# Optimization experiments

Measured on AMD Instinct MI355X. Metric: run time of the kernel, lower is better.

Reference implementation:

```python
import jax, jax.numpy as jnp
import numpy as np

N_NODES = 50000
N_EDGES = 800000
D_IN = 128
D_OUT = 128
D_RED = 32  # out_features // reduction
ORDER = 3


def setup_inputs() -> dict:
    key = jax.random.key(0)
    ks = jax.random.split(key, 16)
    s = 1.0 / np.sqrt(D_IN)
    inp = {
        'features': jax.random.normal(ks[0], (N_NODES, D_IN), jnp.float32),
        'edge_row': jax.random.randint(ks[1], (N_EDGES,), 0, N_NODES, jnp.int32),
        'edge_col': jax.random.randint(ks[2], (N_EDGES,), 0, N_NODES, jnp.int32),
        'edge_val': jax.random.uniform(ks[3], (N_EDGES,), jnp.float32) / 16.0,  # ~1/avg_degree normalization
        'w1': jax.random.normal(ks[4], (D_IN, D_OUT), jnp.float32) * s,
        'b1': jax.random.normal(ks[5], (D_OUT,), jnp.float32) * s,
        'w2': jax.random.normal(ks[6], (D_IN, D_OUT), jnp.float32) * s,
        'b2': jax.random.normal(ks[7], (D_OUT,), jnp.float32) * s,
        'w3': jax.random.normal(ks[8], (D_IN, D_OUT), jnp.float32) * s,
        'b3': jax.random.normal(ks[9], (D_OUT,), jnp.float32) * s,
        'fc1_w': jax.random.normal(ks[10], (D_OUT, D_RED), jnp.float32) * s,
        'fc1_b': jax.random.normal(ks[11], (D_RED,), jnp.float32) * s,
        'fc2_w': jax.random.normal(ks[12], (D_RED, D_OUT), jnp.float32) * (1.0 / np.sqrt(D_RED)),
        'fc2_b': jax.random.normal(ks[13], (D_OUT,), jnp.float32) * s,
    }
    return inp


def reference(features, edge_row, edge_col, edge_val, w1, b1, w2, b2, w3, b3,
              fc1_w, fc1_b, fc2_w, fc2_b):
    def spmm(x):  # sparse [N,N] @ dense [N,D] via gather + segment_sum
        msgs = edge_val[:, None] * x[edge_col]          # [E, D]
        return jax.ops.segment_sum(msgs, edge_row, num_segments=N_NODES)

    def ngnn(w, b, order):
        h = jnp.tanh(features @ w)                      # active=True path
        for _ in range(order):                          # order spmm hops
            h = spmm(h)
        return h + b

    abstract = [ngnn(w, b, k + 1) for k, (w, b) in enumerate([(w1, b1), (w2, b2), (w3, b3)])]
    feats = jnp.stack(abstract, axis=0)                 # [order, N, D]
    m = jnp.mean(feats, axis=1)                         # [order, D]
    a = jax.nn.relu(m @ fc1_w + fc1_b) @ fc2_w + fc2_b  # [order, D]
    a = jax.nn.softmax(a, axis=0)                       # softmax over order dim
    out = jnp.einsum('ond,od->nd', feats, a)            # weighted combine
    return out
```

## Files before the change

kernel.cpp:

```cpp
#include <hip/hip_runtime.h>
#include <cstdint>

#define N_NODES 50000
#define N_EDGES 800000
#define DIM 128
#define EPCAP 64

typedef _Float16 half8 __attribute__((ext_vector_type(8)));
typedef float f32x4 __attribute__((ext_vector_type(4)));


__device__ inline unsigned pack_half2(float lo, float hi) {
    union { _Float16 h[2]; unsigned u; } cv;
    cv.h[0] = (_Float16)lo; cv.h[1] = (_Float16)hi;
    return cv.u;
}
__device__ inline float h_lo(unsigned u) {
    union { unsigned u; _Float16 h[2]; } cv; cv.u = u; return (float)cv.h[0];
}
__device__ inline float h_hi(unsigned u) {
    union { unsigned u; _Float16 h[2]; } cv; cv.u = u; return (float)cv.h[1];
}


__global__ void scatter_kernel(const int* __restrict__ rows, const int* __restrict__ cols,
                               const float* __restrict__ vals, int* __restrict__ cnt,
                               unsigned* __restrict__ ep, int ne) {
    int e = blockIdx.x * blockDim.x + threadIdx.x;
    if (e < ne) {
        int r = rows[e];
        int p = atomicAdd(&cnt[r], 1);
        union { _Float16 h; unsigned short s; } cv; cv.h = (_Float16)vals[e];
        if (p < EPCAP) ep[(size_t)r * EPCAP + p] = ((unsigned)cv.s << 16) | (unsigned)cols[e];
    }
}


__global__ __launch_bounds__(256) void wprep_kernel(const float* __restrict__ w3,
                                                    const float* __restrict__ w2,
                                                    const float* __restrict__ w1,
                                                    _Float16* __restrict__ Wt) {
    const float* W = (blockIdx.x == 0) ? w3 : (blockIdx.x == 1) ? w2 : w1;
    _Float16* O = Wt + (size_t)blockIdx.x * 16384;
    int tid = threadIdx.x;
    for (int i = tid; i < 16384; i += 256) {
        int j = i >> 7, d = i & 127;
        O[j * 128 + d] = (_Float16)W[d * 128 + j];
    }
}


__global__ __launch_bounds__(256) void gemm_mfma3_kernel(const float* __restrict__ F,
                                                         const _Float16* __restrict__ Wt,
                                                         unsigned* __restrict__ T1, int nrows) {
    __shared__ _Float16 Fs[64 * 128];
    __shared__ _Float16 Ws[128 * 128];
    int tid = threadIdx.x;
    int lane = tid & 63, wv = tid >> 6;
    int c = lane & 15, g = lane >> 4;
    int rowbase = blockIdx.x * 64;

    for (int i = tid; i < 4096; i += 256) {
        int r = i >> 6;
        int row = rowbase + r; if (row >= nrows) row = nrows - 1;
        float2 fv = ((const float2*)F)[(size_t)row * 64 + (i & 63)];
        *(unsigned*)((char*)Fs + ((i * 4) ^ ((r & 15) << 4))) = pack_half2(fv.x, fv.y);
    }
    __syncthreads();

    half8 afr[4];
    #pragma unroll
    for (int ks = 0; ks < 4; ++ks) {
        int off = (((wv * 16 + c) * 128 + ks * 32 + g * 8) * 2) ^ (c << 4);
        afr[ks] = *(const half8*)((const char*)Fs + off);
    }

    for (int b = 0; b < 3; ++b) {
        const unsigned* WtU = (const unsigned*)(Wt + (size_t)b * 16384);
        for (int i = tid; i < 8192; i += 256) {
            int j = i >> 6;
            *(unsigned*)((char*)Ws + ((i * 4) ^ ((j & 15) << 4))) = WtU[i];
        }
        __syncthreads();

        f32x4 zero = {0.f, 0.f, 0.f, 0.f};
        f32x4 acc[8];
        #pragma unroll
        for (int t = 0; t < 8; ++t) acc[t] = zero;

        #pragma unroll
        for (int ks = 0; ks < 4; ++ks) {
            #pragma unroll
            for (int t = 0; t < 8; ++t) {
                int j = t * 16 + c;
                int off = ((j * 128 + ks * 32 + g * 8) * 2) ^ ((j & 15) << 4);
                half8 bfr = *(const half8*)((const char*)Ws + off);
                acc[t] = __builtin_amdgcn_mfma_f32_16x16x32_f16(afr[ks], bfr, acc[t], 0, 0, 0);
            }
        }

        #pragma unroll
        for (int t = 0; t < 4; ++t) {
            int j = t * 16 + c;
            #pragma unroll
            for (int r = 0; r < 4; ++r) {
                int row = rowbase + wv * 16 + g * 4 + r;
                if (row < nrows)
                    T1[(size_t)row * 192 + b * 64 + j] =
                        pack_half2(tanhf(acc[t][r]), tanhf(acc[t + 4][r]));
            }
        }
        __syncthreads();
    }
}


template <int NCHUNK, bool F32FINAL>
__global__ __launch_bounds__(512) void spmm_stage_kernel(const int* __restrict__ cnts,
                                                         const unsigned* __restrict__ ep,
                                                         const unsigned* __restrict__ x,
                                                         unsigned* __restrict__ ob0,
                                                         unsigned* __restrict__ obf,
                                                         float* __restrict__ fout,
                                                         float* __restrict__ csum) {
    __shared__ float cs[128];
    int tid = threadIdx.x;
    if (tid < 128) cs[tid] = 0.f;
    __syncthreads();

    int row = blockIdx.x * 8 + (tid >> 6);
    int lane = tid & 63;
    int n = __builtin_amdgcn_readfirstlane(cnts[row]);
    n = n < EPCAP ? n : EPCAP;
    const unsigned* e0 = ep + (size_t)row * EPCAP;

    float ax[NCHUNK], ay[NCHUNK];
    #pragma unroll
    for (int cc = 0; cc < NCHUNK; ++cc) { ax[cc] = 0.f; ay[cc] = 0.f; }

    const unsigned* xl = x + lane;
    constexpr int U = (NCHUNK == 1) ? 8 : 4;
    int i = 0;
    for (; i + U <= n; i += U) {
        unsigned p[U];
        #pragma unroll
        for (int u = 0; u < U; ++u) p[u] = e0[i + u];
        unsigned gx[U][NCHUNK];
        #pragma unroll
        for (int u = 0; u < U; ++u) {
            unsigned b = (p[u] & 0xFFFFu) * (unsigned)(NCHUNK * 64);
            #pragma unroll
            for (int cc = 0; cc < NCHUNK; ++cc) gx[u][cc] = xl[b + cc * 64];
        }
        #pragma unroll
        for (int u = 0; u < U; ++u) {
            union { unsigned short s; _Float16 h; } cu; cu.s = (unsigned short)(p[u] >> 16);
            float v = (float)cu.h;
            #pragma unroll
            for (int cc = 0; cc < NCHUNK; ++cc) {
                ax[cc] += v * h_lo(gx[u][cc]);
                ay[cc] += v * h_hi(gx[u][cc]);
            }
        }
    }
    for (; i < n; ++i) {
        unsigned p = e0[i];
        unsigned b = (p & 0xFFFFu) * (unsigned)(NCHUNK * 64);
        union { unsigned short s; _Float16 h; } cu; cu.s = (unsigned short)(p >> 16);
        float v = (float)cu.h;
        #pragma unroll
        for (int cc = 0; cc < NCHUNK; ++cc) {
            unsigned gg = xl[b + cc * 64];
            ax[cc] += v * h_lo(gg);
            ay[cc] += v * h_hi(gg);
        }
    }

    #pragma unroll
    for (int cc = 0; cc < NCHUNK - 1; ++cc)
        ob0[(size_t)row * ((NCHUNK - 1) * 64) + cc * 64 + lane] = pack_half2(ax[cc], ay[cc]);

    float fx = ax[NCHUNK - 1], fy = ay[NCHUNK - 1];
    if (F32FINAL) {
        fout[(size_t)row * 128 + lane] = fx;
        fout[(size_t)row * 128 + 64 + lane] = fy;
    } else {
        obf[(size_t)row * 64 + lane] = pack_half2(fx, fy);
    }
    atomicAdd(&cs[2 * lane + 0], fx);
    atomicAdd(&cs[2 * lane + 1], fy);
    __syncthreads();
    if (tid < 128) atomicAdd(&csum[(blockIdx.x & 7) * 384 + tid], cs[tid]);
}


__global__ __launch_bounds__(128) void fc_softmax_kernel(const float* __restrict__ csum,
                                                         const float* __restrict__ b1,
                                                         const float* __restrict__ b2,
                                                         const float* __restrict__ b3,
                                                         const float* __restrict__ fc1w,
                                                         const float* __restrict__ fc1b,
                                                         const float* __restrict__ fc2w,
                                                         const float* __restrict__ fc2b,
                                                         float* __restrict__ wgt) {
    __shared__ float m[3][128];
    __shared__ float r[3][32];
    int t = threadIdx.x;
    const float inv = 1.0f / (float)N_NODES;
    int slot = (t < 64) ? (2 * t) : (2 * (t - 64) + 1);
    #pragma unroll
    for (int k = 0; k < 3; ++k) {
        float s = 0.f;
        #pragma unroll
        for (int rep = 0; rep < 8; ++rep) s += csum[rep * 384 + k * 128 + slot];
        const float* bk = (k == 0) ? b1 : (k == 1) ? b2 : b3;
        m[k][t] = s * inv + bk[t];
    }
    __syncthreads();
    if (t < 96) {
        int k = t >> 5, j = t & 31;
        float acc = fc1b[j];
        for (int d = 0; d < 128; ++d) acc += m[k][d] * fc1w[d * 32 + j];
        r[k][j] = fmaxf(acc, 0.f);
    }
    __syncthreads();
    float a[3];
    #pragma unroll
    for (int k = 0; k < 3; ++k) {
        float acc = fc2b[t];
        for (int j = 0; j < 32; ++j) acc += r[k][j] * fc2w[j * 128 + t];
        a[k] = acc;
    }
    float mx = fmaxf(a[0], fmaxf(a[1], a[2]));
    float e0 = expf(a[0] - mx), e1 = expf(a[1] - mx), e2 = expf(a[2] - mx);
    float s = e0 + e1 + e2;
    wgt[0 * 128 + t] = e0 / s;
    wgt[1 * 128 + t] = e1 / s;
    wgt[2 * 128 + t] = e2 / s;
}


__global__ __launch_bounds__(256) void combine_kernel(float* __restrict__ out,
                                                      const unsigned* __restrict__ f2,
                                                      const unsigned* __restrict__ f3,
                                                      const float* __restrict__ b1,
                                                      const float* __restrict__ b2,
                                                      const float* __restrict__ b3,
                                                      const float* __restrict__ wgt) {
    const int total = N_NODES * 32;
    int idx0 = blockIdx.x * blockDim.x + threadIdx.x;
    int stride = gridDim.x * blockDim.x;
    int qb = idx0 & 31;
    float4 W0 = ((const float4*)wgt)[qb];
    float4 W1 = ((const float4*)wgt)[32 + qb];
    float4 W2 = ((const float4*)wgt)[64 + qb];
    float4 B1 = ((const float4*)b1)[qb];
    float4 B2 = ((const float4*)b2)[qb];
    float4 B3 = ((const float4*)b3)[qb];
    bool hi = qb >= 16;
    int qm = qb & 15;
    for (int idx = idx0; idx < total; idx += stride) {
        int row = idx >> 5;
        float4 v1 = ((const float4*)out)[idx];
        uint4 u2 = ((const uint4*)f2)[row * 16 + qm];
        uint4 u3 = ((const uint4*)f3)[row * 16 + qm];
        float f2x = hi ? h_hi(u2.x) : h_lo(u2.x);
        float f2y = hi ? h_hi(u2.y) : h_lo(u2.y);
        float f2z = hi ? h_hi(u2.z) : h_lo(u2.z);
        float f2w = hi ? h_hi(u2.w) : h_lo(u2.w);
        float f3x = hi ? h_hi(u3.x) : h_lo(u3.x);
        float f3y = hi ? h_hi(u3.y) : h_lo(u3.y);
        float f3z = hi ? h_hi(u3.z) : h_lo(u3.z);
        float f3w = hi ? h_hi(u3.w) : h_lo(u3.w);
        float4 o;
        o.x = (v1.x + B1.x) * W0.x + (f2x + B2.x) * W1.x + (f3x + B3.x) * W2.x;
        o.y = (v1.y + B1.y) * W0.y + (f2y + B2.y) * W1.y + (f3y + B3.y) * W2.y;
        o.z = (v1.z + B1.z) * W0.z + (f2z + B2.z) * W1.z + (f3z + B3.z) * W2.z;
        o.w = (v1.w + B1.w) * W0.w + (f2w + B2.w) * W1.w + (f3w + B3.w) * W2.w;
        ((float4*)out)[idx] = o;
    }
}


extern "C" void kernel_launch(void* const* d_in, const int* in_sizes, int n_in,
                              void* d_out, int out_size, void* d_ws, size_t ws_size,
                              hipStream_t stream) {
    const float* F    = (const float*)d_in[0];
    const int*   erow = (const int*)d_in[1];
    const int*   ecol = (const int*)d_in[2];
    const float* eval_ = (const float*)d_in[3];
    const float* w1 = (const float*)d_in[4];  const float* b1 = (const float*)d_in[5];
    const float* w2 = (const float*)d_in[6];  const float* b2 = (const float*)d_in[7];
    const float* w3 = (const float*)d_in[8];  const float* b3 = (const float*)d_in[9];
    const float* fc1w = (const float*)d_in[10]; const float* fc1b = (const float*)d_in[11];
    const float* fc2w = (const float*)d_in[12]; const float* fc2b = (const float*)d_in[13];
    float* out = (float*)d_out;

    char* ws = (char*)d_ws;
    size_t off = 0;
    auto alloc = [&](size_t bytes) -> void* {
        off = (off + 255) & ~(size_t)255;
        void* p = ws + off;
        off += bytes;
        return p;
    };
    unsigned* T1   = (unsigned*)alloc((size_t)N_NODES * 192 * 4);
    unsigned* T2   = (unsigned*)alloc((size_t)N_NODES * 128 * 4);
    unsigned* T3   = (unsigned*)alloc((size_t)N_NODES * 64 * 4);
    unsigned* ep   = (unsigned*)alloc((size_t)N_NODES * EPCAP * 4);
    int*   counts  = (int*)alloc((size_t)N_NODES * sizeof(int));
    _Float16* Wt   = (_Float16*)alloc(3 * 16384 * sizeof(_Float16));
    float* csum    = (float*)alloc(8 * 3 * 128 * sizeof(float));
    float* wgt     = (float*)alloc(3 * 128 * sizeof(float));
    unsigned* f2bf = T1;
    unsigned* f3bf = T1 + (size_t)N_NODES * 64;

    hipMemsetAsync(counts, 0, (size_t)N_NODES * sizeof(int), stream);
    hipMemsetAsync(csum, 0, 8 * 3 * 128 * sizeof(float), stream);

    scatter_kernel<<<(N_EDGES + 255) / 256, 256, 0, stream>>>(erow, ecol, eval_, counts, ep, N_EDGES);
    wprep_kernel<<<3, 256, 0, stream>>>(w3, w2, w1, Wt);
    gemm_mfma3_kernel<<<(N_NODES + 63) / 64, 256, 0, stream>>>(F, Wt, T1, N_NODES);

    const int spmmGrid = N_NODES / 8;

    spmm_stage_kernel<3, true><<<spmmGrid, 512, 0, stream>>>(counts, ep, T1, T2,
                                                             nullptr, out, csum + 0 * 128);
    spmm_stage_kernel<2, false><<<spmmGrid, 512, 0, stream>>>(counts, ep, T2, T3,
                                                              f2bf, nullptr, csum + 1 * 128);
    spmm_stage_kernel<1, false><<<spmmGrid, 512, 0, stream>>>(counts, ep, T3, nullptr,
                                                              f3bf, nullptr, csum + 2 * 128);

    fc_softmax_kernel<<<1, 128, 0, stream>>>(csum, b1, b2, b3, fc1w, fc1b, fc2w, fc2b, wgt);
    combine_kernel<<<2048, 256, 0, stream>>>(out, f2bf, f3bf, b1, b2, b3, wgt);
}
```

Before: 345.4 us.

## Interleave SpMM feature chunks per lane and fuse small setup kernels

Changes the T1 layout so each lane's three (and two) chunks sit next to each other, letting SpMM gathers use one vector load per edge instead of several strided loads. Unroll is raised to 8 for all stages. The scatter kernel is fused with the weight-transpose kernel using nontemporal stores, the two memsets are merged into one, and the fc/softmax step is folded into every combine block. The fold makes each of the 2048 blocks redo the tiny MLP, which adds redundant work in exchange for fewer launches.

```diff
diff --git a/kernel.cpp b/kernel.cpp
--- a/kernel.cpp
+++ b/kernel.cpp
@@ -23,30 +23,33 @@
 }
 
 
-__global__ void scatter_kernel(const int* __restrict__ rows, const int* __restrict__ cols,
-                               const float* __restrict__ vals, int* __restrict__ cnt,
-                               unsigned* __restrict__ ep, int ne) {
-    int e = blockIdx.x * blockDim.x + threadIdx.x;
-    if (e < ne) {
-        int r = rows[e];
-        int p = atomicAdd(&cnt[r], 1);
-        union { _Float16 h; unsigned short s; } cv; cv.h = (_Float16)vals[e];
-        if (p < EPCAP) ep[(size_t)r * EPCAP + p] = ((unsigned)cv.s << 16) | (unsigned)cols[e];
-    }
-}
-
-
-__global__ __launch_bounds__(256) void wprep_kernel(const float* __restrict__ w3,
-                                                    const float* __restrict__ w2,
-                                                    const float* __restrict__ w1,
-                                                    _Float16* __restrict__ Wt) {
-    const float* W = (blockIdx.x == 0) ? w3 : (blockIdx.x == 1) ? w2 : w1;
-    _Float16* O = Wt + (size_t)blockIdx.x * 16384;
-    int tid = threadIdx.x;
-    for (int i = tid; i < 16384; i += 256) {
-        int j = i >> 7, d = i & 127;
-        O[j * 128 + d] = (_Float16)W[d * 128 + j];
-    }
+__global__ __launch_bounds__(256) void scatter_wprep_kernel(const int* __restrict__ rows,
+                                                            const int* __restrict__ cols,
+                                                            const float* __restrict__ vals,
+                                                            int* __restrict__ cnt,
+                                                            unsigned* __restrict__ ep,
+                                                            const float* __restrict__ w3,
+                                                            const float* __restrict__ w2,
+                                                            const float* __restrict__ w1,
+                                                            _Float16* __restrict__ Wt) {
+    int bx = blockIdx.x;
+    if (bx >= 3125) {
+        int b = bx - 3125;
+        const float* W = (b == 0) ? w3 : (b == 1) ? w2 : w1;
+        _Float16* O = Wt + (size_t)b * 16384;
+        for (int i = threadIdx.x; i < 16384; i += 256) {
+            int j = i >> 7, d = i & 127;
+            O[j * 128 + d] = (_Float16)W[d * 128 + j];
+        }
+        return;
+    }
+    int e = bx * 256 + threadIdx.x;
+    int r = rows[e];
+    int p = atomicAdd(&cnt[r], 1);
+    union { _Float16 h; unsigned short s; } cv; cv.h = (_Float16)vals[e];
+    if (p < EPCAP)
+        __builtin_nontemporal_store(((unsigned)cv.s << 16) | (unsigned)cols[e],
+                                    &ep[(size_t)r * EPCAP + p]);
 }
 
 
@@ -106,7 +109,7 @@
             for (int r = 0; r < 4; ++r) {
                 int row = rowbase + wv * 16 + g * 4 + r;
                 if (row < nrows)
-                    T1[(size_t)row * 192 + b * 64 + j] =
+                    T1[(size_t)row * 192 + j * 3 + b] =
                         pack_half2(tanhf(acc[t][r]), tanhf(acc[t + 4][r]));
             }
         }
@@ -138,19 +141,26 @@
     #pragma unroll
     for (int cc = 0; cc < NCHUNK; ++cc) { ax[cc] = 0.f; ay[cc] = 0.f; }
 
-    const unsigned* xl = x + lane;
-    constexpr int U = (NCHUNK == 1) ? 8 : 4;
+    const unsigned* xl = x + lane * NCHUNK;
+    constexpr int U = 8;
     int i = 0;
     for (; i + U <= n; i += U) {
         unsigned p[U];
         #pragma unroll
         for (int u = 0; u < U; ++u) p[u] = e0[i + u];
-        unsigned gx[U][NCHUNK];
+        unsigned g[U][NCHUNK];
         #pragma unroll
         for (int u = 0; u < U; ++u) {
-            unsigned b = (p[u] & 0xFFFFu) * (unsigned)(NCHUNK * 64);
-            #pragma unroll
-            for (int cc = 0; cc < NCHUNK; ++cc) gx[u][cc] = xl[b + cc * 64];
+            size_t b = (size_t)(p[u] & 0xFFFFu) * (NCHUNK * 64);
+            if constexpr (NCHUNK == 3) {
+                uint3 v = *(const uint3*)(xl + b);
+                g[u][0] = v.x; g[u][1] = v.y; g[u][2] = v.z;
+            } else if constexpr (NCHUNK == 2) {
+                uint2 v = *(const uint2*)(xl + b);
+                g[u][0] = v.x; g[u][1] = v.y;
+            } else {
+                g[u][0] = xl[b];
+            }
         }
         #pragma unroll
         for (int u = 0; u < U; ++u) {
@@ -158,27 +168,32 @@
             float v = (float)cu.h;
             #pragma unroll
             for (int cc = 0; cc < NCHUNK; ++cc) {
-                ax[cc] += v * h_lo(gx[u][cc]);
-                ay[cc] += v * h_hi(gx[u][cc]);
+                ax[cc] += v * h_lo(g[u][cc]);
+                ay[cc] += v * h_hi(g[u][cc]);
             }
         }
     }
     for (; i < n; ++i) {
         unsigned p = e0[i];
-        unsigned b = (p & 0xFFFFu) * (unsigned)(NCHUNK * 64);
+        size_t b = (size_t)(p & 0xFFFFu) * (NCHUNK * 64);
         union { unsigned short s; _Float16 h; } cu; cu.s = (unsigned short)(p >> 16);
         float v = (float)cu.h;
         #pragma unroll
         for (int cc = 0; cc < NCHUNK; ++cc) {
-            unsigned gg = xl[b + cc * 64];
+            unsigned gg = xl[b + cc];
             ax[cc] += v * h_lo(gg);
             ay[cc] += v * h_hi(gg);
         }
     }
 
-    #pragma unroll
-    for (int cc = 0; cc < NCHUNK - 1; ++cc)
-        ob0[(size_t)row * ((NCHUNK - 1) * 64) + cc * 64 + lane] = pack_half2(ax[cc], ay[cc]);
+    if constexpr (NCHUNK == 3) {
+        uint2 o;
+        o.x = pack_half2(ax[0], ay[0]);
+        o.y = pack_half2(ax[1], ay[1]);
+        *(uint2*)(ob0 + (size_t)row * 128 + lane * 2) = o;
+    } else if constexpr (NCHUNK == 2) {
+        ob0[(size_t)row * 64 + lane] = pack_half2(ax[0], ay[0]);
+    }
 
     float fx = ax[NCHUNK - 1], fy = ay[NCHUNK - 1];
     if (F32FINAL) {
@@ -194,66 +209,66 @@
 }
 
 
-__global__ __launch_bounds__(128) void fc_softmax_kernel(const float* __restrict__ csum,
-                                                         const float* __restrict__ b1,
-                                                         const float* __restrict__ b2,
-                                                         const float* __restrict__ b3,
-                                                         const float* __restrict__ fc1w,
-                                                         const float* __restrict__ fc1b,
-                                                         const float* __restrict__ fc2w,
-                                                         const float* __restrict__ fc2b,
-                                                         float* __restrict__ wgt) {
+__global__ __launch_bounds__(256) void combine_kernel(float* __restrict__ out,
+                                                      const unsigned* __restrict__ f2,
+                                                      const unsigned* __restrict__ f3,
+                                                      const float* __restrict__ csum,
+                                                      const float* __restrict__ b1,
+                                                      const float* __restrict__ b2,
+                                                      const float* __restrict__ b3,
+                                                      const float* __restrict__ fc1w,
+                                                      const float* __restrict__ fc1b,
+                                                      const float* __restrict__ fc2w,
+                                                      const float* __restrict__ fc2b) {
     __shared__ float m[3][128];
-    __shared__ float r[3][32];
+    __shared__ float rr[3][32];
+    __shared__ float wgt[3][128];
     int t = threadIdx.x;
-    const float inv = 1.0f / (float)N_NODES;
-    int slot = (t < 64) ? (2 * t) : (2 * (t - 64) + 1);
-    #pragma unroll
-    for (int k = 0; k < 3; ++k) {
-        float s = 0.f;
-        #pragma unroll
-        for (int rep = 0; rep < 8; ++rep) s += csum[rep * 384 + k * 128 + slot];
-        const float* bk = (k == 0) ? b1 : (k == 1) ? b2 : b3;
-        m[k][t] = s * inv + bk[t];
+
+    if (t < 128) {
+        const float inv = 1.0f / (float)N_NODES;
+        int slot = (t < 64) ? (2 * t) : (2 * (t - 64) + 1);
+        #pragma unroll
+        for (int k = 0; k < 3; ++k) {
+            float s = 0.f;
+            #pragma unroll
+            for (int rep = 0; rep < 8; ++rep) s += csum[rep * 384 + k * 128 + slot];
+            const float* bk = (k == 0) ? b1 : (k == 1) ? b2 : b3;
+            m[k][t] = s * inv + bk[t];
+        }
     }
     __syncthreads();
     if (t < 96) {
         int k = t >> 5, j = t & 31;
         float acc = fc1b[j];
         for (int d = 0; d < 128; ++d) acc += m[k][d] * fc1w[d * 32 + j];
-        r[k][j] = fmaxf(acc, 0.f);
-    }
-    __syncthreads();
-    float a[3];
-    #pragma unroll
-    for (int k = 0; k < 3; ++k) {
-        float acc = fc2b[t];
-        for (int j = 0; j < 32; ++j) acc += r[k][j] * fc2w[j * 128 + t];
-        a[k] = acc;
-    }
-    float mx = fmaxf(a[0], fmaxf(a[1], a[2]));
-    float e0 = expf(a[0] - mx), e1 = expf(a[1] - mx), e2 = expf(a[2] - mx);
-    float s = e0 + e1 + e2;
-    wgt[0 * 128 + t] = e0 / s;
-    wgt[1 * 128 + t] = e1 / s;
-    wgt[2 * 128 + t] = e2 / s;
-}
-
-
-__global__ __launch_bounds__(256) void combine_kernel(float* __restrict__ out,
-                                                      const unsigned* __restrict__ f2,
-                                                      const unsigned* __restrict__ f3,
-                                                      const float* __restrict__ b1,
-                                                      const float* __restrict__ b2,
-                                                      const float* __restrict__ b3,
-                                                      const float* __restrict__ wgt) {
+        rr[k][j] = fmaxf(acc, 0.f);
+    }
+    __syncthreads();
+    if (t < 128) {
+        float a[3];
+        #pragma unroll
+        for (int k = 0; k < 3; ++k) {
+            float acc = fc2b[t];
+            for (int j = 0; j < 32; ++j) acc += rr[k][j] * fc2w[j * 128 + t];
+            a[k] = acc;
+        }
+        float mx = fmaxf(a[0], fmaxf(a[1], a[2]));
+        float e0 = expf(a[0] - mx), e1 = expf(a[1] - mx), e2 = expf(a[2] - mx);
+        float s = e0 + e1 + e2;
+        wgt[0][t] = e0 / s;
+        wgt[1][t] = e1 / s;
+        wgt[2][t] = e2 / s;
+    }
+    __syncthreads();
+
     const int total = N_NODES * 32;
     int idx0 = blockIdx.x * blockDim.x + threadIdx.x;
     int stride = gridDim.x * blockDim.x;
     int qb = idx0 & 31;
-    float4 W0 = ((const float4*)wgt)[qb];
-    float4 W1 = ((const float4*)wgt)[32 + qb];
-    float4 W2 = ((const float4*)wgt)[64 + qb];
+    float4 W0 = *(const float4*)&wgt[0][qb * 4];
+    float4 W1 = *(const float4*)&wgt[1][qb * 4];
+    float4 W2 = *(const float4*)&wgt[2][qb * 4];
     float4 B1 = ((const float4*)b1)[qb];
     float4 B2 = ((const float4*)b2)[qb];
     float4 B3 = ((const float4*)b3)[qb];
@@ -309,17 +324,16 @@
     unsigned* T3   = (unsigned*)alloc((size_t)N_NODES * 64 * 4);
     unsigned* ep   = (unsigned*)alloc((size_t)N_NODES * EPCAP * 4);
     int*   counts  = (int*)alloc((size_t)N_NODES * sizeof(int));
+    float* csum    = (float*)alloc(8 * 3 * 128 * sizeof(float));
     _Float16* Wt   = (_Float16*)alloc(3 * 16384 * sizeof(_Float16));
-    float* csum    = (float*)alloc(8 * 3 * 128 * sizeof(float));
-    float* wgt     = (float*)alloc(3 * 128 * sizeof(float));
     unsigned* f2bf = T1;
     unsigned* f3bf = T1 + (size_t)N_NODES * 64;
 
-    hipMemsetAsync(counts, 0, (size_t)N_NODES * sizeof(int), stream);
-    hipMemsetAsync(csum, 0, 8 * 3 * 128 * sizeof(float), stream);
-
-    scatter_kernel<<<(N_EDGES + 255) / 256, 256, 0, stream>>>(erow, ecol, eval_, counts, ep, N_EDGES);
-    wprep_kernel<<<3, 256, 0, stream>>>(w3, w2, w1, Wt);
+    size_t zlen = (size_t)((char*)csum + 8 * 3 * 128 * sizeof(float) - (char*)counts);
+    hipMemsetAsync(counts, 0, zlen, stream);
+
+    scatter_wprep_kernel<<<3125 + 3, 256, 0, stream>>>(erow, ecol, eval_, counts, ep,
+                                                       w3, w2, w1, Wt);
     gemm_mfma3_kernel<<<(N_NODES + 63) / 64, 256, 0, stream>>>(F, Wt, T1, N_NODES);
 
     const int spmmGrid = N_NODES / 8;
@@ -331,6 +345,6 @@
     spmm_stage_kernel<1, false><<<spmmGrid, 512, 0, stream>>>(counts, ep, T3, nullptr,
                                                               f3bf, nullptr, csum + 2 * 128);
 
-    fc_softmax_kernel<<<1, 128, 0, stream>>>(csum, b1, b2, b3, fc1w, fc1b, fc2w, fc2b, wgt);
-    combine_kernel<<<2048, 256, 0, stream>>>(out, f2bf, f3bf, b1, b2, b3, wgt);
-}
+    combine_kernel<<<2048, 256, 0, stream>>>(out, f2bf, f3bf, csum, b1, b2, b3,
+                                             fc1w, fc1b, fc2w, fc2b);
+}
```

Result: slower. 367.1 us (+6.3%).
